# Performance work log

Measured on AMD Instinct MI355X. Metric: run time of the kernel, lower is better.

Reference implementation:

```python
import jax, jax.numpy as jnp
from jax import lax
import numpy as np

K = 32          # points per ball
RADIUS = 0.2    # ball radius
SCALE = 2       # downsampling factor


def setup_inputs() -> dict:
    key = jax.random.key(0)
    k1, k2 = jax.random.split(key)
    xyz = jax.random.normal(k1, (4, 8192, 3), jnp.float32)
    feats = jax.random.normal(k2, (4, 64, 8192), jnp.float32)
    return {"xyz": xyz, "feats": feats}


def furthest_point_sample(xyz, m):
    """xyz: (bs, n, 3) -> idx (bs, m) int32. Matches PointNet++ CUDA FPS (seed = point 0)."""
    bs, n, _ = xyz.shape

    def body(carry, _):
        min_d2, last_idx = carry                                  # (bs,n), (bs,)
        last = jnp.take_along_axis(xyz, last_idx[:, None, None], axis=1)  # (bs,1,3)
        d2 = jnp.sum((xyz - last) ** 2, axis=-1)                  # (bs,n)
        min_d2 = jnp.minimum(min_d2, d2)
        nxt = jnp.argmax(min_d2, axis=-1).astype(jnp.int32)
        return (min_d2, nxt), last_idx

    init = (jnp.full((bs, n), 1e10, xyz.dtype), jnp.zeros((bs,), jnp.int32))
    _, idxs = lax.scan(body, init, None, length=m)                # (m, bs)
    return idxs.T                                                 # (bs, m)


def ball_query(xyz, child_xyz, radius, k):
    """First-k-within-radius neighbor search.
    xyz: (bs,n,3), child_xyz: (bs,m,3) -> idx (bs,m,k) int32, filled (bs,m,k) bool.
    Empty slots are padded with the first valid index (or 0 if ball is empty),
    matching the CUDA ball_query semantics."""
    n = xyz.shape[1]
    d2 = jnp.sum((child_xyz[:, :, None, :] - xyz[:, None, :, :]) ** 2, axis=-1)  # (bs,m,n)
    mask = d2 <= radius * radius
    # score: larger = earlier valid index; 0 = invalid. top_k then yields the
    # first k in-radius indices in ascending index order.
    score = jnp.where(mask, n - jnp.arange(n, dtype=jnp.int32), 0)  # (bs,m,n)
    vals, idx = lax.top_k(score, k)                                 # (bs,m,k)
    filled = vals > 0
    first = idx[..., 0:1]
    idx = jnp.where(filled, idx, first).astype(jnp.int32)
    return idx, filled


def reference(xyz, feats):
    bs, n, _ = xyz.shape
    c = feats.shape[1]
    m = n // SCALE

    # --- furthest point sampling + gather child coordinates ---
    child_idx = furthest_point_sample(xyz, m)                       # (bs,m)
    child_xyz = jnp.take_along_axis(xyz, child_idx[:, :, None], axis=1)  # (bs,m,3)

    # --- ball query + group features ---
    idx, filled = ball_query(xyz, child_xyz, RADIUS, K)             # (bs,m,K)
    grouped = jnp.take_along_axis(
        feats, idx.reshape(bs, 1, m * K), axis=2
    ).reshape(bs, c, m, K)                                          # (bs,c,m,K)

    # --- max pool over the ball ---
    child_feats = jnp.max(grouped, axis=-1)                         # (bs,c,m)
    return child_xyz, child_feats
```

## Files before the change

### kernel.cpp

```cpp
#include <hip/hip_runtime.h>
#include <cstdint>

#define N_PTS 8192
#define M_PTS 4096
#define BS 4
#define CH 64
#define KNN 32
#define R2D (0.2 * 0.2)

template <int CTRL, int RM>
__device__ __forceinline__ float dppmax(float v) {
  int s = __builtin_amdgcn_update_dpp(__float_as_int(v), __float_as_int(v),
                                      CTRL, RM, 0xf, false);
  return fmaxf(v, __int_as_float(s));
}
__device__ __forceinline__ float readlane_f(float v, int l) {
  return __int_as_float(__builtin_amdgcn_readlane(__float_as_int(v), l));
}

__global__ __launch_bounds__(1024, 4) void fps_kernel(const float* __restrict__ xyz,
                                                      float* __restrict__ child_xyz) {
  __shared__ float  sx[N_PTS], sy[N_PTS], sz[N_PTS];
  __shared__ float  scomb[2][64];
  __shared__ double sbv[2][16];
  __shared__ int    sbi[2][16];

  const int b = blockIdx.x;
  const int t = threadIdx.x;
  const int lane = t & 63;
  const int wid  = t >> 6;
  const float* p = xyz + (size_t)b * N_PTS * 3;

  for (int e = t; e < N_PTS * 3; e += 1024) {
    float v = p[e];
    int i = e / 3, k = e - i * 3;
    if (k == 0) sx[i] = v; else if (k == 1) sy[i] = v; else sz[i] = v;
  }
  __syncthreads();

  double px[8], py[8], pz[8], md[8];
#pragma unroll
  for (int q = 0; q < 8; ++q) {
    int i = t + (q << 10);
    px[q] = (double)sx[i]; py[q] = (double)sy[i]; pz[q] = (double)sz[i];
    md[q] = 1e10;
  }
#pragma unroll
  for (int q = 0; q < 8; ++q) {
    asm volatile("" : "+v"(px[q]), "+v"(py[q]), "+v"(pz[q]));
  }

  double bv = -1.0; int bi = 0; float proxy = -1.0f;
  bool iwon = false;
  float cx_c = 0.f, cy_c = 0.f, cz_c = 0.f;

  float lx = sx[0], ly = sy[0], lz = sz[0];

  for (int it = 0; it < M_PTS; ++it) {
    if (t == 0) {
      float* o = child_xyz + ((size_t)b * M_PTS + it) * 3;
      o[0] = lx; o[1] = ly; o[2] = lz;
    }
    const double lxd = (double)lx, lyd = (double)ly, lzd = (double)lz;

    bool changed = false;
#pragma unroll
    for (int q = 0; q < 8; ++q) {
      double dx = px[q] - lxd, dy = py[q] - lyd, dz = pz[q] - lzd;
      double d2 = dx * dx + dy * dy + dz * dz;
      bool c = d2 < md[q];
      md[q] = c ? d2 : md[q];
      changed |= c;
    }

    if (__any(changed)) {
      bv = md[0];
#pragma unroll
      for (int q = 1; q < 8; ++q) bv = fmax(bv, md[q]);
      bi = 0x7fffffff;
#pragma unroll
      for (int q = 7; q >= 0; --q) if (md[q] == bv) bi = t + (q << 10);
      proxy = (float)bv;

      float v = proxy;
      v = dppmax<0x111, 0xf>(v);
      v = dppmax<0x112, 0xf>(v);
      v = dppmax<0x114, 0xf>(v);
      v = dppmax<0x118, 0xf>(v);
      v = dppmax<0x142, 0xa>(v);
      v = dppmax<0x143, 0xc>(v);
      const float wmax = readlane_f(v, 63);

      const unsigned long long m = __ballot(proxy == wmax);
      bool iwon_now;
      if (__popcll(m) == 1) {
        iwon_now = (lane == (int)(__ffsll(m) - 1));
      } else {
        double tv = bv; int ti = bi;
#pragma unroll
        for (int off = 32; off; off >>= 1) {
          double ov = __shfl_xor(tv, off);
          int    oi = __shfl_xor(ti, off);
          if (ov > tv || (ov == tv && oi < ti)) { tv = ov; ti = oi; }
        }
        iwon_now = (bv == tv) && (bi == ti);
      }
      iwon = iwon_now;
      if (iwon) { cx_c = sx[bi]; cy_c = sy[bi]; cz_c = sz[bi]; }
    }

    const int pb = it & 1;
    if (iwon) {
      scomb[pb][wid]      = proxy;
      scomb[pb][16 + wid] = cx_c;
      scomb[pb][32 + wid] = cy_c;
      scomb[pb][48 + wid] = cz_c;
      sbv[pb][wid] = bv; sbi[pb][wid] = bi;
    }
    __syncthreads();

    const float cval = scomb[pb][lane];
    float r = cval;
    r = dppmax<0x111, 0xf>(r);
    r = dppmax<0x112, 0xf>(r);
    r = dppmax<0x114, 0xf>(r);
    r = dppmax<0x118, 0xf>(r);
    const float gmax = readlane_f(r, 15);
    const unsigned long long gm = __ballot((lane < 16) && (cval == gmax));
    int w;
    if (__popcll(gm) == 1) {
      w = (int)(__ffsll(gm) - 1);
    } else {
      double bestv = -1.0; int besti = 0x7fffffff; w = 0;
      for (int ww = 0; ww < 16; ++ww) if ((gm >> ww) & 1) {
        double vv = sbv[pb][ww]; int ii = sbi[pb][ww];
        if (vv > bestv || (vv == bestv && ii < besti)) { bestv = vv; besti = ii; w = ww; }
      }
    }
    const int ws = __builtin_amdgcn_readfirstlane(w);
    lx = readlane_f(cval, 16 + ws);
    ly = readlane_f(cval, 32 + ws);
    lz = readlane_f(cval, 48 + ws);
  }
}

__global__ __launch_bounds__(256) void transpose_kernel(const float* __restrict__ feats,
                                                        float* __restrict__ featsT) {
  __shared__ float tile[CH][65];
  const int b = blockIdx.y;
  const int i0 = blockIdx.x * 64;
  const int t = threadIdx.x;
  const float* src = feats + (size_t)b * CH * N_PTS;
#pragma unroll
  for (int r = 0; r < 16; ++r) {
    int e = t + r * 256;
    int c = e >> 6, ii = e & 63;
    tile[c][ii] = src[(size_t)c * N_PTS + i0 + ii];
  }
  __syncthreads();
  float* dst = featsT + ((size_t)b * N_PTS + i0) * CH;
#pragma unroll
  for (int r = 0; r < 16; ++r) {
    int e = t + r * 256;
    int ii = e >> 6, c = e & 63;
    dst[(size_t)ii * CH + c] = tile[c][ii];
  }
}

__global__ __launch_bounds__(1024) void ballgroup_kernel(const float* __restrict__ xyz,
                                                         const float* __restrict__ child_xyz,
                                                         const float* __restrict__ featsrc,
                                                         float* __restrict__ child_feats,
                                                         int useT) {
  __shared__ float sx[N_PTS], sy[N_PTS], sz[N_PTS];
  __shared__ int slist[16][KNN];
  const int b = blockIdx.y;
  const int t = threadIdx.x;
  const int lane = t & 63, wid = t >> 6;
  const float* p = xyz + (size_t)b * N_PTS * 3;
  for (int e = t; e < N_PTS * 3; e += 1024) {
    float v = p[e];
    int i = e / 3, k = e - i * 3;
    if (k == 0) sx[i] = v; else if (k == 1) sy[i] = v; else sz[i] = v;
  }
  __syncthreads();

  const int j = blockIdx.x * 16 + wid;
  const float* cc = child_xyz + ((size_t)b * M_PTS + j) * 3;
  const double cx = (double)cc[0], cy = (double)cc[1], cz = (double)cc[2];

  int taken = 0;
  for (int i0 = 0; i0 < N_PTS && taken < KNN; i0 += 64) {
    const int i = i0 + lane;
    double dx = cx - (double)sx[i], dy = cy - (double)sy[i], dz = cz - (double)sz[i];
    double d2 = dx * dx + dy * dy + dz * dz;
    const bool hit = d2 <= R2D;
    const unsigned long long msk = __ballot(hit);
    if (msk) {
      int slot = taken + __popcll(msk & ((1ull << lane) - 1ull));
      if (hit && slot < KNN) slist[wid][slot] = i;
      taken += (int)__popcll(msk);
    }
  }
  int cnt = taken < KNN ? taken : KNN;
  if (cnt == 0) { if (lane == 0) slist[wid][0] = 0; cnt = 1; }

  float acc = -INFINITY;
  for (int q = 0; q < cnt; ++q) {
    const int idx = slist[wid][q];
    float v = useT ? featsrc[((size_t)b * N_PTS + idx) * CH + lane]
                   : featsrc[((size_t)b * CH + lane) * N_PTS + idx];
    acc = fmaxf(acc, v);
  }
  child_feats[((size_t)b * CH + lane) * M_PTS + j] = acc;
}

extern "C" void kernel_launch(void* const* d_in, const int* in_sizes, int n_in,
                              void* d_out, int out_size, void* d_ws, size_t ws_size,
                              hipStream_t stream) {
  const float* xyz   = (const float*)d_in[0];
  const float* feats = (const float*)d_in[1];
  float* out = (float*)d_out;
  float* child_xyz   = out;
  float* child_feats = out + (size_t)BS * M_PTS * 3;
  float* featsT = (float*)d_ws;
  const int useT = ws_size >= (size_t)BS * N_PTS * CH * sizeof(float);

  fps_kernel<<<BS, 1024, 0, stream>>>(xyz, child_xyz);
  if (useT) transpose_kernel<<<dim3(N_PTS / 64, BS), 256, 0, stream>>>(feats, featsT);
  ballgroup_kernel<<<dim3(M_PTS / 16, BS), 1024, 0, stream>>>(
      xyz, child_xyz, useT ? featsT : feats, child_feats, useT);
}
```

Before: 4.758 ms.

## Sort FPS points by Morton code and skip clusters beyond current max distance

Before the FPS loop, points are quantized, Morton-encoded and bitonic-sorted in shared memory so that each wave's 64-point chunks form spatial clusters with a centroid and bounding radius. On each iteration a cluster's min-distance update is skipped when the cluster lies farther from the newly selected point than the current global max distance plus its radius. The aim is to cut the per-iteration distance work in the serial FPS loop. This adds a one-time sort, extra register state and divergence, and correctness depends on the conservative float bounds and on index tie-breaking now using original indices.

```diff
diff --git a/kernel.cpp b/kernel.cpp
--- a/kernel.cpp
+++ b/kernel.cpp
@@ -7,6 +7,7 @@
 #define CH 64
 #define KNN 32
 #define R2D (0.2 * 0.2)
+#define NCL 128
 
 template <int CTRL, int RM>
 __device__ __forceinline__ float dppmax(float v) {
@@ -18,12 +19,23 @@
   return __int_as_float(__builtin_amdgcn_readlane(__float_as_int(v), l));
 }
 
+__device__ __forceinline__ uint32_t part3(uint32_t x) {
+  x &= 0x3FF;
+  x = (x | (x << 16)) & 0x030000FF;
+  x = (x | (x << 8))  & 0x0300F00F;
+  x = (x | (x << 4))  & 0x030C30C3;
+  x = (x | (x << 2))  & 0x09249249;
+  return x;
+}
+
 __global__ __launch_bounds__(1024, 4) void fps_kernel(const float* __restrict__ xyz,
                                                       float* __restrict__ child_xyz) {
-  __shared__ float  sx[N_PTS], sy[N_PTS], sz[N_PTS];
-  __shared__ float  scomb[2][64];
-  __shared__ double sbv[2][16];
-  __shared__ int    sbi[2][16];
+  __shared__ float    sx[N_PTS], sy[N_PTS], sz[N_PTS];
+  __shared__ uint32_t skey[N_PTS];
+  __shared__ float    sclx[NCL], scly[NCL], sclz[NCL], sclr[NCL];
+  __shared__ float    scomb[2][64];
+  __shared__ double   sbv[2][16];
+  __shared__ int      sbi[2][16];
 
   const int b = blockIdx.x;
   const int t = threadIdx.x;
@@ -38,22 +50,66 @@
   }
   __syncthreads();
 
-  double px[8], py[8], pz[8], md[8];
+  for (int i = t; i < N_PTS; i += 1024) {
+    uint32_t qx = (uint32_t)min(63, max(0, (int)((sx[i] + 8.0f) * 4.0f)));
+    uint32_t qy = (uint32_t)min(63, max(0, (int)((sy[i] + 8.0f) * 4.0f)));
+    uint32_t qz = (uint32_t)min(63, max(0, (int)((sz[i] + 8.0f) * 4.0f)));
+    uint32_t mc = part3(qx) | (part3(qy) << 1) | (part3(qz) << 2);
+    skey[i] = (mc << 13) | (uint32_t)i;
+  }
+  __syncthreads();
+
+  for (int k = 2; k <= N_PTS; k <<= 1) {
+    for (int j = k >> 1; j > 0; j >>= 1) {
+      for (int i = t; i < N_PTS; i += 1024) {
+        int ixj = i ^ j;
+        if (ixj > i) {
+          uint32_t a = skey[i], c = skey[ixj];
+          if (((i & k) == 0) ? (a > c) : (a < c)) { skey[i] = c; skey[ixj] = a; }
+        }
+      }
+      __syncthreads();
+    }
+  }
+
+  float pxf[8], pyf[8], pzf[8];
+  int   oi[8];
+  double md[8];
 #pragma unroll
   for (int q = 0; q < 8; ++q) {
-    int i = t + (q << 10);
-    px[q] = (double)sx[i]; py[q] = (double)sy[i]; pz[q] = (double)sz[i];
+    const int c = wid * 8 + q;
+    const int idx = (int)(skey[c * 64 + lane] & 0x1FFFu);
+    oi[q] = idx;
+    pxf[q] = sx[idx]; pyf[q] = sy[idx]; pzf[q] = sz[idx];
     md[q] = 1e10;
-  }
-#pragma unroll
-  for (int q = 0; q < 8; ++q) {
-    asm volatile("" : "+v"(px[q]), "+v"(py[q]), "+v"(pz[q]));
+    float cxs = pxf[q], cys = pyf[q], czs = pzf[q];
+#pragma unroll
+    for (int off = 32; off; off >>= 1) {
+      cxs += __shfl_xor(cxs, off); cys += __shfl_xor(cys, off); czs += __shfl_xor(czs, off);
+    }
+    cxs *= (1.0f / 64.0f); cys *= (1.0f / 64.0f); czs *= (1.0f / 64.0f);
+    float dx = pxf[q] - cxs, dy = pyf[q] - cys, dz = pzf[q] - czs;
+    float r2 = dx * dx + dy * dy + dz * dz;
+#pragma unroll
+    for (int off = 32; off; off >>= 1) r2 = fmaxf(r2, __shfl_xor(r2, off));
+    if (lane == 0) {
+      sclx[c] = cxs; scly[c] = cys; sclz[c] = czs;
+      sclr[c] = sqrtf(r2) * 1.0002f + 1e-5f;
+    }
+  }
+  __syncthreads();
+
+  float ccx_r = 0.f, ccy_r = 0.f, ccz_r = 0.f, crad_r = 0.f;
+  if (lane < 8) {
+    const int c = wid * 8 + lane;
+    ccx_r = sclx[c]; ccy_r = scly[c]; ccz_r = sclz[c]; crad_r = sclr[c];
   }
 
   double bv = -1.0; int bi = 0; float proxy = -1.0f;
   bool iwon = false;
   float cx_c = 0.f, cy_c = 0.f, cz_c = 0.f;
 
+  float gmaxf = 3.0e38f;
   float lx = sx[0], ly = sy[0], lz = sz[0];
 
   for (int it = 0; it < M_PTS; ++it) {
@@ -63,14 +119,23 @@
     }
     const double lxd = (double)lx, lyd = (double)ly, lzd = (double)lz;
 
+    const float sg = sqrtf(gmaxf * 1.000002f + 1e-30f) * 1.000001f + 1e-4f;
+    float dxc = ccx_r - lx, dyc = ccy_r - ly, dzc = ccz_r - lz;
+    float d2c = dxc * dxc + dyc * dyc + dzc * dzc;
+    float thr = crad_r + sg;
+    bool need = !(d2c * 0.99999f >= thr * thr);
+    const unsigned long long updm = __ballot((lane < 8) && need);
+
     bool changed = false;
 #pragma unroll
     for (int q = 0; q < 8; ++q) {
-      double dx = px[q] - lxd, dy = py[q] - lyd, dz = pz[q] - lzd;
-      double d2 = dx * dx + dy * dy + dz * dz;
-      bool c = d2 < md[q];
-      md[q] = c ? d2 : md[q];
-      changed |= c;
+      if ((updm >> q) & 1ull) {
+        double dx = (double)pxf[q] - lxd, dy = (double)pyf[q] - lyd, dz = (double)pzf[q] - lzd;
+        double d2 = dx * dx + dy * dy + dz * dz;
+        bool c = d2 < md[q];
+        md[q] = c ? d2 : md[q];
+        changed |= c;
+      }
     }
 
     if (__any(changed)) {
@@ -79,7 +144,7 @@
       for (int q = 1; q < 8; ++q) bv = fmax(bv, md[q]);
       bi = 0x7fffffff;
 #pragma unroll
-      for (int q = 7; q >= 0; --q) if (md[q] == bv) bi = t + (q << 10);
+      for (int q = 0; q < 8; ++q) if (md[q] == bv && oi[q] < bi) bi = oi[q];
       proxy = (float)bv;
 
       float v = proxy;
@@ -100,8 +165,8 @@
 #pragma unroll
         for (int off = 32; off; off >>= 1) {
           double ov = __shfl_xor(tv, off);
-          int    oi = __shfl_xor(ti, off);
-          if (ov > tv || (ov == tv && oi < ti)) { tv = ov; ti = oi; }
+          int    oib = __shfl_xor(ti, off);
+          if (ov > tv || (ov == tv && oib < ti)) { tv = ov; ti = oib; }
         }
         iwon_now = (bv == tv) && (bi == ti);
       }
@@ -141,6 +206,7 @@
     lx = readlane_f(cval, 16 + ws);
     ly = readlane_f(cval, 32 + ws);
     lz = readlane_f(cval, 48 + ws);
+    gmaxf = gmax;
   }
 }
 
```

Result: faster. 4.447 ms (-6.5%).
